# Kernel optimization log

Hardware: AMD Instinct MI355X
Metric: run time of the kernel (lower is better)

## Reference

```python
import jax, jax.numpy as jnp
import numpy as np
from jax import lax

THRESHOLD = 0.9


def _conv(x, w, b, stride):
    # x: [B,C,H,W], w: [O,I,3,3] (OIHW)
    y = lax.conv_general_dilated(x, w, (stride, stride), 'SAME',
                                 dimension_numbers=('NCHW', 'OIHW', 'NCHW'))
    return y + b[None, :, None, None]


def _expert(x, w1, b1, w2, b2, wf, bf):
    h = jax.nn.relu(_conv(x, w1, b1, 2))   # [B,64,112,112]
    h = jax.nn.relu(_conv(h, w2, b2, 2))   # [B,128,56,56]
    g = h.mean(axis=(2, 3))                # [B,128] global average pool
    return g @ wf + bf                     # [B,2] logits


def setup_inputs() -> dict:
    key = jax.random.key(0)
    ks = jax.random.split(key, 13)
    f32 = jnp.float32
    def rn(k, shape, scale):
        return jax.random.normal(k, shape, dtype=f32) * scale
    return {
        'x':    rn(ks[0], (64, 3, 224, 224), 1.0),
        't_w1': rn(ks[1], (64, 3, 3, 3),   0.2),
        't_b1': jnp.zeros((64,), f32),
        't_w2': rn(ks[2], (128, 64, 3, 3), 0.05),
        't_b2': jnp.zeros((128,), f32),
        't_wf': rn(ks[3], (128, 2),        0.1),
        't_bf': jnp.zeros((2,), f32),
        'f_w1': rn(ks[4], (64, 3, 3, 3),   0.2),
        'f_b1': jnp.zeros((64,), f32),
        'f_w2': rn(ks[5], (128, 64, 3, 3), 0.05),
        'f_b2': jnp.zeros((128,), f32),
        'f_wf': rn(ks[6], (128, 2),        0.1),
        'f_bf': jnp.zeros((2,), f32),
    }


def reference(x, t_w1, t_b1, t_w2, t_b2, t_wf, t_bf,
              f_w1, f_b1, f_w2, f_b2, f_wf, f_bf):
    t_logits = _expert(x, t_w1, t_b1, t_w2, t_b2, t_wf, t_bf)   # [B,2]
    t_conf = jax.nn.softmax(t_logits, axis=1).max(axis=1)        # [B]
    use_texture2 = t_conf <= THRESHOLD                           # [B] bool
    # jit-friendly dense evaluation of the second expert; the where-mask
    # reproduces the original gather/scatter blend exactly (values and grads).
    f_logits = _expert(x, f_w1, f_b1, f_w2, f_b2, f_wf, f_bf)   # [B,2]
    output = jnp.where(use_texture2[:, None],
                       0.7 * t_logits + 0.3 * f_logits,
                       t_logits)
    freq_usage = use_texture2.astype(jnp.float32).mean()
    return (output, freq_usage)
```

## Files before the change

kernel.cpp:

```cpp
#include <hip/hip_runtime.h>
#include <hip/hip_fp16.h>
#include <math.h>


#define W2B_OFF   0ull
#define W1F_OFF   294912ull
#define G_OFF     303104ull
#define H1_OFF    368640ull
#define H1E_US    52301824ull
#define H1B_US    817216ull
#define WS_NEED   (H1_OFF + 2ull*H1E_US*2ull + 4096ull)

typedef __attribute__((ext_vector_type(8))) short bf16x8;
typedef __attribute__((ext_vector_type(8))) _Float16 half8;
typedef __attribute__((ext_vector_type(4))) float f32x4;

__device__ inline ushort f2h(float v) {
  __half h = __float2half(v);
  return *(ushort*)&h;
}

__global__ __launch_bounds__(256) void prep_new(
    const float* __restrict__ w2_t, const float* __restrict__ w2_f,
    const float* __restrict__ w1_t, const float* __restrict__ w1_f,
    char* __restrict__ ws) {
  int idx = blockIdx.x * 256 + threadIdx.x;
  ushort* w2frag = (ushort*)(ws + W2B_OFF);
  ushort* w1frag = (ushort*)(ws + W1F_OFF);
  if (idx < 147456) {
    int j    = idx & 7;
    int lane = (idx >> 3) & 63;
    int t2   = idx >> 9;
    int kc   = t2 % 18;
    int t3   = t2 / 18;
    int octile = t3 & 7;
    int e    = t3 >> 3;
    int oc = octile * 16 + (lane & 15);
    int kk = kc * 32 + (lane >> 4) * 8 + j;
    int kh = kk / 192, r2 = kk - kh * 192, kw = r2 >> 6, slot = r2 & 63;
    int icp = ((slot >> 2) & 3) * 16 + ((slot >> 4) & 3) * 4 + (slot & 3);
    const float* src = e ? w2_f : w2_t;
    w2frag[idx] = f2h(src[((oc * 64 + icp) * 3 + kh) * 3 + kw]);
  } else if (idx < 147456 + 4096) {
    int i2   = idx - 147456;
    int j    = i2 & 7;
    int lane = (i2 >> 3) & 63;
    int m    = (i2 >> 9) & 3;
    int e    = (i2 >> 11) & 1;
    int oc = m * 16 + (lane & 15);
    int kk = (lane >> 4) * 8 + j;
    const float* src = e ? w1_f : w1_t;
    w1frag[i2] = f2h((kk < 27) ? src[oc * 27 + kk] : 0.f);
  }
}

__global__ __launch_bounds__(256) void conv1_mfma(
    const float* __restrict__ x,
    const ushort* __restrict__ w1f_all,
    const float* __restrict__ b1_t, const float* __restrict__ b1_f,
    ushort* __restrict__ h1_all)
{
  const int gR  = blockIdx.x;
  const int b   = blockIdx.y;
  const int e   = blockIdx.z;
  const int tid = threadIdx.x;
  const int w    = tid >> 6;
  const int lane = tid & 63;
  const int q    = lane >> 4;
  const int n    = lane & 15;

  ushort* h1b = h1_all + (size_t)e * H1E_US + (size_t)b * H1B_US;
  const float* b1 = e ? b1_f : b1_t;

  constexpr int CW = 233;
  __shared__ unsigned int xs[3 * 9 * CW];

  const float* xb = x + (size_t)b * 150528;
  const int xr0 = 8 * gR;
  for (int i = tid; i < 1512; i += 256) {
    int ic  = i / 504;
    int rem = i - ic * 504;
    int r   = rem / 56;
    int u   = rem - r * 56;
    int xr  = xr0 + r;
    float4 p = make_float4(0.f, 0.f, 0.f, 0.f);
    if (xr < 224) p = *(const float4*)(xb + (ic * 224 + xr) * 224 + 4 * u);
    int base = (ic * 9 + r) * CW + 4 * u;
    xs[base + 0] = (unsigned int)f2h(p.x);
    xs[base + 1] = (unsigned int)f2h(p.y);
    xs[base + 2] = (unsigned int)f2h(p.z);
    xs[base + 3] = (unsigned int)f2h(p.w);
  }
  if (tid < 27) xs[tid * CW + 224] = 0;

  h1b[((size_t)((4 * gR + (tid >> 6)) * 113 + 112)) * 64 + (tid & 63)] = 0;
  if (gR == 0) {
    unsigned int* z = (unsigned int*)&h1b[(size_t)112 * 113 * 64];
    for (int i = tid; i < 3616; i += 256) z[i] = 0;
  }

  half8 wf[4];
#pragma unroll
  for (int m = 0; m < 4; ++m)
    wf[m] = *(const half8*)&w1f_all[(((size_t)(e * 4 + m)) * 64 + lane) * 8];
  float4 bv[4];
#pragma unroll
  for (int m = 0; m < 4; ++m)
    bv[m] = *(const float4*)&b1[m * 16 + 4 * q];

  int off[8];
#pragma unroll
  for (int j = 0; j < 8; ++j) {
    int kk = q * 8 + j;
    if (kk < 27) {
      int ic = kk / 9;
      int r9 = kk - ic * 9;
      int kh = r9 / 3;
      int kw = r9 - kh * 3;
      off[j] = (ic * 9 + kh) * CW + kw;
    } else {
      off[j] = -1;
    }
  }

  __syncthreads();

  const int row   = 4 * gR + w;
  const int rbase = (2 * w) * CW;

  for (int nt = 0; nt < 7; ++nt) {
    const int c = nt * 16 + n;
    const int base = rbase + 2 * c;
    unsigned int g[8];
#pragma unroll
    for (int j = 0; j < 8; ++j)
      g[j] = (off[j] >= 0) ? xs[base + off[j]] : 0u;
    union { half8 h; unsigned int u[4]; } bh;
#pragma unroll
    for (int p = 0; p < 4; ++p)
      bh.u[p] = (g[2 * p] & 0xffffu) | (g[2 * p + 1] << 16);
    f32x4 acc[4];
#pragma unroll
    for (int m = 0; m < 4; ++m) acc[m] = (f32x4){0.f, 0.f, 0.f, 0.f};
#pragma unroll
    for (int m = 0; m < 4; ++m)
      acc[m] = __builtin_amdgcn_mfma_f32_16x16x32_f16(wf[m], bh.h, acc[m], 0, 0, 0);
    size_t po = ((size_t)(row * 113 + c)) * 64 + q * 16;
    union { ushort us[16]; uint4 v4[2]; } pk;
#pragma unroll
    for (int m = 0; m < 4; ++m) {
      pk.us[m * 4 + 0] = f2h(fmaxf(acc[m][0] + bv[m].x, 0.f));
      pk.us[m * 4 + 1] = f2h(fmaxf(acc[m][1] + bv[m].y, 0.f));
      pk.us[m * 4 + 2] = f2h(fmaxf(acc[m][2] + bv[m].z, 0.f));
      pk.us[m * 4 + 3] = f2h(fmaxf(acc[m][3] + bv[m].w, 0.f));
    }
    *(uint4*)&h1b[po]     = pk.v4[0];
    *(uint4*)&h1b[po + 8] = pk.v4[1];
  }
}

__global__ __launch_bounds__(256) void conv2_mfma(
    const ushort* __restrict__ h1_all,
    const ushort* __restrict__ w2frag,
    const float* __restrict__ b2_t, const float* __restrict__ b2_f,
    float* __restrict__ g)
{
  const int T = blockIdx.x;
  const int b = blockIdx.y;
  const int e = blockIdx.z;
  const int tid  = threadIdx.x;
  const int w    = tid >> 6;
  const int lane = tid & 63;
  const ushort* h1b = h1_all + (size_t)e * H1E_US + (size_t)b * H1B_US;
  const float* b2 = e ? b2_f : b2_t;

  __shared__ ushort hs[5 * 113 * 64];

  const int q   = lane >> 4;
  const int n   = lane & 15;
  const int pxl = lane & 7;
  const int rl  = (lane >> 3) & 1;

#pragma unroll
  for (int half = 0; half < 2; ++half) {
    bf16x8 tmp[9];
    int dst[9];
    bool ok[9];
#pragma unroll
    for (int k = 0; k < 9; ++k) {
      int s = tid + (half * 9 + k) * 256;
      ok[k] = (s < 4520);
      int r = s / 904;
      int rem = s - 904 * r;
      int hx = rem >> 3, gq = rem & 7;
      if (ok[k])
        tmp[k] = *(const bf16x8*)&h1b[((size_t)((4 * T + r) * 113 + hx)) * 64 + 8 * gq];
      dst[k] = (r * 113 + hx) * 64 + 8 * (gq ^ (hx & 7));
    }
#pragma unroll
    for (int k = 0; k < 9; ++k)
      if (ok[k]) *(bf16x8*)&hs[dst[k]] = tmp[k];
  }
  __syncthreads();

  f32x4 acc[2][7];
#pragma unroll
  for (int mt = 0; mt < 2; ++mt)
#pragma unroll
    for (int nt = 0; nt < 7; ++nt) acc[mt][nt] = (f32x4){0.f, 0.f, 0.f, 0.f};

  for (int kh = 0; kh < 3; ++kh) {
    const int rbase = (kh + 2 * rl) * 113 * 64;
#pragma unroll
    for (int kw = 0; kw < 3; ++kw) {
#pragma unroll
      for (int icc = 0; icc < 2; ++icc) {
        const int kc = kh * 6 + kw * 2 + icc;
        const int gsw = 8 * ((icc * 4 + q) ^ ((2 * pxl + kw) & 7));
        half8 bf[7];
#pragma unroll
        for (int nt = 0; nt < 7; ++nt) {
          int hx = 2 * (8 * nt + pxl) + kw;
          bf[nt] = *(const half8*)&hs[rbase + hx * 64 + gsw];
        }
#pragma unroll
        for (int mt = 0; mt < 2; ++mt) {
          const int octile = 2 * w + mt;
          half8 af = *(const half8*)
              &w2frag[((size_t)((e * 8 + octile) * 18 + kc)) * 512 + lane * 8];
#pragma unroll
          for (int nt = 0; nt < 7; ++nt)
            acc[mt][nt] = __builtin_amdgcn_mfma_f32_16x16x32_f16(
                af, bf[nt], acc[mt][nt], 0, 0, 0);
        }
      }
    }
  }

#pragma unroll
  for (int mt = 0; mt < 2; ++mt) {
#pragma unroll
    for (int reg = 0; reg < 4; ++reg) {
      const int oc = 32 * w + 16 * mt + 4 * q + reg;
      const float bias = b2[oc];
      float s = 0.f;
#pragma unroll
      for (int nt = 0; nt < 7; ++nt) s += fmaxf(acc[mt][nt][reg] + bias, 0.f);
      s += __shfl_xor(s, 1);
      s += __shfl_xor(s, 2);
      s += __shfl_xor(s, 4);
      s += __shfl_xor(s, 8);
      if (n == 0) atomicAdd(&g[((size_t)e * 64 + b) * 128 + oc], s);
    }
  }
}

__global__ __launch_bounds__(64) void finale(
    const float* __restrict__ g,
    const float* __restrict__ t_wf, const float* __restrict__ t_bf,
    const float* __restrict__ f_wf, const float* __restrict__ f_bf,
    float* __restrict__ out)
{
  const int b = threadIdx.x;
  const float inv = 1.0f / 3136.0f;
  const float* gt = g + b * 128;
  const float* gf = g + (64 + b) * 128;
  float lt0 = t_bf[0], lt1 = t_bf[1];
  float lf0 = f_bf[0], lf1 = f_bf[1];
  for (int k = 0; k < 128; ++k) {
    float vt = gt[k] * inv;
    float vf = gf[k] * inv;
    lt0 = fmaf(vt, t_wf[2 * k],     lt0);
    lt1 = fmaf(vt, t_wf[2 * k + 1], lt1);
    lf0 = fmaf(vf, f_wf[2 * k],     lf0);
    lf1 = fmaf(vf, f_wf[2 * k + 1], lf1);
  }
  float m  = fmaxf(lt0, lt1);
  float e0 = expf(lt0 - m), e1 = expf(lt1 - m);
  float conf = fmaxf(e0, e1) / (e0 + e1);
  bool use2 = (conf <= 0.9f);
  out[2 * b]     = use2 ? 0.7f * lt0 + 0.3f * lf0 : lt0;
  out[2 * b + 1] = use2 ? 0.7f * lt1 + 0.3f * lf1 : lt1;
  unsigned long long mask = __ballot(use2);
  if (b == 0) out[128] = (float)__popcll(mask) * (1.0f / 64.0f);
}

__global__ __launch_bounds__(256) void transpose_w2(
    const float* __restrict__ w2_t, const float* __restrict__ w2_f,
    float* __restrict__ w2t) {
  int idx = blockIdx.x * 256 + threadIdx.x;
  int e = idx / 73728;
  int r = idx - e * 73728;
  int k = r >> 7, oc = r & 127;
  const float* src = e ? w2_f : w2_t;
  w2t[idx] = src[oc * 576 + k];
}

__global__ __launch_bounds__(256, 3) void fused_expert(
    const float* __restrict__ x,
    const float* __restrict__ w1_t, const float* __restrict__ b1_t,
    const float* __restrict__ b2_t,
    const float* __restrict__ w1_f, const float* __restrict__ b1_f,
    const float* __restrict__ b2_f,
    const float* __restrict__ w2t_all, float* __restrict__ g)
{
  const int tile = blockIdx.x, b = blockIdx.y, e = blockIdx.z;
  const int ty = tile >> 1, tx = tile & 1;
  const float* w1  = e ? w1_f : w1_t;
  const float* b1  = e ? b1_f : b1_t;
  const float* b2  = e ? b2_f : b2_t;
  const float* w2t = w2t_all + e * 73728;
  __shared__ float x_s[3 * 19 * 116];
  __shared__ float h1_s[8 * 9 * 58];
  __shared__ float w1_s[1728];
  const int tid = threadIdx.x;
  {
    const float* xb = x + (size_t)b * 150528;
    const int xr0 = ty * 16, xc0 = tx * 112;
    for (int idx = tid; idx < 3 * 19 * 116; idx += 256) {
      int ic = idx / (19 * 116);
      int rem = idx - ic * (19 * 116);
      int r = rem / 116, cc = rem - r * 116;
      int xr = xr0 + r, xc = xc0 + cc;
      float v = 0.f;
      if (xr < 224 && xc < 224 && cc < 115) v = xb[(ic * 224 + xr) * 224 + xc];
      x_s[idx] = v;
    }
    for (int idx = tid; idx < 1728; idx += 256) w1_s[idx] = w1[idx];
  }
  const int ocg = tid >> 4, posg = tid & 15;
  int pbase[7];
#pragma unroll
  for (int j = 0; j < 7; ++j) {
    int p = posg + 16 * j, py = p / 28, px = p - py * 28;
    pbase[j] = py * 2 * 58 + px * 2;
  }
  float acc[7][8];
#pragma unroll
  for (int j = 0; j < 7; ++j)
#pragma unroll
    for (int i = 0; i < 8; ++i) acc[j][i] = 0.f;
  const int hc_l = tid >> 5, l32 = tid & 31;
  for (int c = 0; c < 8; ++c) {
    __syncthreads();
    {
      const int hc = c * 8 + hc_l;
      const float bias = b1[hc];
      float wr[27];
#pragma unroll
      for (int qq = 0; qq < 27; ++qq) wr[qq] = w1_s[hc * 27 + qq];
      for (int p = l32; p < 513; p += 32) {
        int hy = p / 57, hx = p - hy * 57;
        float a = bias;
#pragma unroll
        for (int ic = 0; ic < 3; ++ic)
#pragma unroll
          for (int kh = 0; kh < 3; ++kh) {
            const float* row = &x_s[ic * (19 * 116) + (2 * hy + kh) * 116 + 2 * hx];
            a = fmaf(row[0], wr[ic * 9 + kh * 3 + 0], a);
            a = fmaf(row[1], wr[ic * 9 + kh * 3 + 1], a);
            a = fmaf(row[2], wr[ic * 9 + kh * 3 + 2], a);
          }
        float v = fmaxf(a, 0.f);
        int hy_g = ty * 8 + hy, hx_g = tx * 56 + hx;
        if (hy_g >= 112 || hx_g >= 112) v = 0.f;
        h1_s[hc_l * 522 + hy * 58 + hx] = v;
      }
    }
    __syncthreads();
    for (int ic_l = 0; ic_l < 8; ++ic_l) {
#pragma unroll
      for (int kh = 0; kh < 3; ++kh)
#pragma unroll
        for (int kw = 0; kw < 3; ++kw) {
          const int k = (c * 8 + ic_l) * 9 + kh * 3 + kw;
          const float4 wA = *(const float4*)(w2t + k * 128 + ocg * 8);
          const float4 wB = *(const float4*)(w2t + k * 128 + ocg * 8 + 4);
          const float* hp = &h1_s[ic_l * 522 + kh * 58 + kw];
#pragma unroll
          for (int j = 0; j < 7; ++j) {
            float h = hp[pbase[j]];
            acc[j][0] = fmaf(wA.x, h, acc[j][0]);
            acc[j][1] = fmaf(wA.y, h, acc[j][1]);
            acc[j][2] = fmaf(wA.z, h, acc[j][2]);
            acc[j][3] = fmaf(wA.w, h, acc[j][3]);
            acc[j][4] = fmaf(wB.x, h, acc[j][4]);
            acc[j][5] = fmaf(wB.y, h, acc[j][5]);
            acc[j][6] = fmaf(wB.z, h, acc[j][6]);
            acc[j][7] = fmaf(wB.w, h, acc[j][7]);
          }
        }
    }
  }
  __syncthreads();
  float* red = x_s;
#pragma unroll
  for (int i = 0; i < 8; ++i) {
    float bb = b2[ocg * 8 + i];
    float t = 0.f;
#pragma unroll
    for (int j = 0; j < 7; ++j) t += fmaxf(acc[j][i] + bb, 0.f);
    red[posg * 129 + ocg * 8 + i] = t;
  }
  __syncthreads();
  if (tid < 128) {
    float t = 0.f;
#pragma unroll
    for (int pg = 0; pg < 16; ++pg) t += red[pg * 129 + tid];
    atomicAdd(&g[(e * 64 + b) * 128 + tid], t);
  }
}

extern "C" void kernel_launch(void* const* d_in, const int* in_sizes, int n_in,
                              void* d_out, int out_size, void* d_ws, size_t ws_size,
                              hipStream_t stream) {
  const float* x    = (const float*)d_in[0];
  const float* t_w1 = (const float*)d_in[1];
  const float* t_b1 = (const float*)d_in[2];
  const float* t_w2 = (const float*)d_in[3];
  const float* t_b2 = (const float*)d_in[4];
  const float* t_wf = (const float*)d_in[5];
  const float* t_bf = (const float*)d_in[6];
  const float* f_w1 = (const float*)d_in[7];
  const float* f_b1 = (const float*)d_in[8];
  const float* f_w2 = (const float*)d_in[9];
  const float* f_b2 = (const float*)d_in[10];
  const float* f_wf = (const float*)d_in[11];
  const float* f_bf = (const float*)d_in[12];
  float* out = (float*)d_out;
  char* ws = (char*)d_ws;

  if (ws_size >= WS_NEED) {
    float*  gbuf   = (float*)(ws + G_OFF);
    ushort* h1     = (ushort*)(ws + H1_OFF);
    ushort* w2frag = (ushort*)(ws + W2B_OFF);
    ushort* w1f    = (ushort*)(ws + W1F_OFF);
    hipMemsetAsync(gbuf, 0, 2 * 64 * 128 * sizeof(float), stream);
    prep_new<<<592, 256, 0, stream>>>(t_w2, f_w2, t_w1, f_w1, ws);
    conv1_mfma<<<dim3(28, 64, 2), 256, 0, stream>>>(x, w1f, t_b1, f_b1, h1);
    conv2_mfma<<<dim3(28, 64, 2), 256, 0, stream>>>(h1, w2frag, t_b2, f_b2, gbuf);
    finale<<<1, 64, 0, stream>>>(gbuf, t_wf, t_bf, f_wf, f_bf, out);
  } else {
    float* w2t = (float*)ws;
    float* g2  = (float*)(ws + 589824);
    hipMemsetAsync(g2, 0, 2 * 64 * 128 * sizeof(float), stream);
    transpose_w2<<<576, 256, 0, stream>>>(t_w2, f_w2, w2t);
    fused_expert<<<dim3(28, 64, 2), 256, 0, stream>>>(
        x, t_w1, t_b1, t_b2, f_w1, f_b1, f_b2, w2t, g2);
    finale<<<1, 64, 0, stream>>>(g2, t_wf, t_bf, f_wf, f_bf, out);
  }
}
```

Before: 245.4 us.

## Split conv2 tiles by column halves and fold gbuf zeroing into prep

Each conv2 block now covers half of the output columns, which shrinks the shared-memory tile to 5x57x64 and the accumulators to 2x4. The launch grid doubles and launch_bounds asks for 4 blocks per CU, aiming at higher occupancy and better latency hiding. The last N tile is only half valid, so lanes past the edge are masked with zeros, which wastes some MFMA work. The global-pool buffer is now zeroed inside prep_new, removing the separate hipMemsetAsync call.

Measured after the change: 274.7 us. 1.12x slower.

```diff
diff --git a/kernel.cpp b/kernel.cpp
--- a/kernel.cpp
+++ b/kernel.cpp
@@ -51,6 +51,8 @@
     int kk = (lane >> 4) * 8 + j;
     const float* src = e ? w1_f : w1_t;
     w1frag[i2] = f2h((kk < 27) ? src[oc * 27 + kk] : 0.f);
+  } else if (idx < 147456 + 4096 + 16384) {
+    ((float*)(ws + G_OFF))[idx - 151552] = 0.f;
   }
 }
 
@@ -159,13 +161,15 @@
   }
 }
 
-__global__ __launch_bounds__(256) void conv2_mfma(
+__global__ __launch_bounds__(256, 4) void conv2_mfma(
     const ushort* __restrict__ h1_all,
     const ushort* __restrict__ w2frag,
     const float* __restrict__ b2_t, const float* __restrict__ b2_f,
     float* __restrict__ g)
 {
-  const int T = blockIdx.x;
+  const int H = blockIdx.x;
+  const int T = H >> 1;
+  const int half = H & 1;
   const int b = blockIdx.y;
   const int e = blockIdx.z;
   const int tid  = threadIdx.x;
@@ -174,62 +178,58 @@
   const ushort* h1b = h1_all + (size_t)e * H1E_US + (size_t)b * H1B_US;
   const float* b2 = e ? b2_f : b2_t;
 
-  __shared__ ushort hs[5 * 113 * 64];
+  __shared__ ushort hs[5 * 57 * 64];
 
   const int q   = lane >> 4;
   const int n   = lane & 15;
   const int pxl = lane & 7;
   const int rl  = (lane >> 3) & 1;
-
-#pragma unroll
-  for (int half = 0; half < 2; ++half) {
-    bf16x8 tmp[9];
-    int dst[9];
-    bool ok[9];
-#pragma unroll
-    for (int k = 0; k < 9; ++k) {
-      int s = tid + (half * 9 + k) * 256;
-      ok[k] = (s < 4520);
-      int r = s / 904;
-      int rem = s - 904 * r;
-      int hx = rem >> 3, gq = rem & 7;
-      if (ok[k])
-        tmp[k] = *(const bf16x8*)&h1b[((size_t)((4 * T + r) * 113 + hx)) * 64 + 8 * gq];
-      dst[k] = (r * 113 + hx) * 64 + 8 * (gq ^ (hx & 7));
-    }
-#pragma unroll
-    for (int k = 0; k < 9; ++k)
-      if (ok[k]) *(bf16x8*)&hs[dst[k]] = tmp[k];
+  const int c0  = 56 * half;
+
+  for (int i = tid; i < 2280; i += 256) {
+    int r   = i / 456;
+    int rem = i - 456 * r;
+    int hl  = rem >> 3;
+    int gq  = rem & 7;
+    int R   = 4 * T + r;
+    *(bf16x8*)&hs[(r * 57 + hl) * 64 + 8 * (gq ^ (hl & 7))] =
+        *(const bf16x8*)&h1b[((size_t)(R * 113 + c0 + hl)) * 64 + 8 * gq];
   }
   __syncthreads();
 
-  f32x4 acc[2][7];
+  f32x4 acc[2][4];
 #pragma unroll
   for (int mt = 0; mt < 2; ++mt)
 #pragma unroll
-    for (int nt = 0; nt < 7; ++nt) acc[mt][nt] = (f32x4){0.f, 0.f, 0.f, 0.f};
-
+    for (int nt = 0; nt < 4; ++nt) acc[mt][nt] = (f32x4){0.f, 0.f, 0.f, 0.f};
+
+  const bool lv3 = (pxl < 4);
+
+#pragma unroll
   for (int kh = 0; kh < 3; ++kh) {
-    const int rbase = (kh + 2 * rl) * 113 * 64;
+    const int rbase = (kh + 2 * rl) * 57 * 64;
 #pragma unroll
     for (int kw = 0; kw < 3; ++kw) {
 #pragma unroll
       for (int icc = 0; icc < 2; ++icc) {
         const int kc = kh * 6 + kw * 2 + icc;
-        const int gsw = 8 * ((icc * 4 + q) ^ ((2 * pxl + kw) & 7));
-        half8 bf[7];
-#pragma unroll
-        for (int nt = 0; nt < 7; ++nt) {
-          int hx = 2 * (8 * nt + pxl) + kw;
-          bf[nt] = *(const half8*)&hs[rbase + hx * 64 + gsw];
+        half8 bf[4];
+#pragma unroll
+        for (int nt = 0; nt < 4; ++nt) {
+          int pxL = 8 * nt + pxl;
+          int hl  = 2 * pxL + kw;
+          if (nt == 3 && !lv3) hl = 0;
+          int gsw = 8 * ((icc * 4 + q) ^ (hl & 7));
+          half8 v = *(const half8*)&hs[rbase + hl * 64 + gsw];
+          if (nt == 3 && !lv3) v = (half8)(_Float16)0.f;
+          bf[nt] = v;
         }
 #pragma unroll
         for (int mt = 0; mt < 2; ++mt) {
-          const int octile = 2 * w + mt;
           half8 af = *(const half8*)
-              &w2frag[((size_t)((e * 8 + octile) * 18 + kc)) * 512 + lane * 8];
-#pragma unroll
-          for (int nt = 0; nt < 7; ++nt)
+              &w2frag[((size_t)((e * 8 + 2 * w + mt) * 18 + kc)) * 512 + lane * 8];
+#pragma unroll
+          for (int nt = 0; nt < 4; ++nt)
             acc[mt][nt] = __builtin_amdgcn_mfma_f32_16x16x32_f16(
                 af, bf[nt], acc[mt][nt], 0, 0, 0);
         }
@@ -245,7 +245,8 @@
       const float bias = b2[oc];
       float s = 0.f;
 #pragma unroll
-      for (int nt = 0; nt < 7; ++nt) s += fmaxf(acc[mt][nt][reg] + bias, 0.f);
+      for (int nt = 0; nt < 3; ++nt) s += fmaxf(acc[mt][nt][reg] + bias, 0.f);
+      if (lv3) s += fmaxf(acc[mt][3][reg] + bias, 0.f);
       s += __shfl_xor(s, 1);
       s += __shfl_xor(s, 2);
       s += __shfl_xor(s, 4);
@@ -435,10 +436,9 @@
     ushort* h1     = (ushort*)(ws + H1_OFF);
     ushort* w2frag = (ushort*)(ws + W2B_OFF);
     ushort* w1f    = (ushort*)(ws + W1F_OFF);
-    hipMemsetAsync(gbuf, 0, 2 * 64 * 128 * sizeof(float), stream);
-    prep_new<<<592, 256, 0, stream>>>(t_w2, f_w2, t_w1, f_w1, ws);
+    prep_new<<<656, 256, 0, stream>>>(t_w2, f_w2, t_w1, f_w1, ws);
     conv1_mfma<<<dim3(28, 64, 2), 256, 0, stream>>>(x, w1f, t_b1, f_b1, h1);
-    conv2_mfma<<<dim3(28, 64, 2), 256, 0, stream>>>(h1, w2frag, t_b2, f_b2, gbuf);
+    conv2_mfma<<<dim3(56, 64, 2), 256, 0, stream>>>(h1, w2frag, t_b2, f_b2, gbuf);
     finale<<<1, 64, 0, stream>>>(gbuf, t_wf, t_bf, f_wf, f_bf, out);
   } else {
     float* w2t = (float*)ws;
```
